# Kernel optimization log

Hardware: AMD Instinct MI355X
Metric: run time of the kernel (lower is better)

## Reference

```python
import jax, jax.numpy as jnp
import numpy as np

B, L, E = 2, 2048, 1024
H = 16
DH = E // H  # head dim for qk and v (dim_qk=dim_v=embed_dim)
HID = 4 * E  # fcn_dim_factor * dim_v
SCALE = DH ** 0.5


def setup_inputs() -> dict:
    key = jax.random.key(0)
    ks = jax.random.split(key, 12)
    s = lambda fan_in: 1.0 / np.sqrt(fan_in)
    return {
        "x": jax.random.uniform(ks[0], (B, L), jnp.float32),
        "z": jax.random.normal(ks[1], (B, L, E), jnp.float32),
        "Wq": jax.random.normal(ks[2], (E, E), jnp.float32) * s(E),
        "bq": jnp.zeros((E,), jnp.float32),
        "Wk": jax.random.normal(ks[3], (E, E), jnp.float32) * s(E),
        "bk": jnp.zeros((E,), jnp.float32),
        "Wv": jax.random.normal(ks[4], (E, E), jnp.float32) * s(E),
        "bv": jnp.zeros((E,), jnp.float32),
        "W1": jax.random.normal(ks[5], (E, HID), jnp.float32) * s(E),
        "b1": jnp.zeros((HID,), jnp.float32),
        "W2": jax.random.normal(ks[6], (HID, 1), jnp.float32) * s(HID),
        "b2": jnp.zeros((1,), jnp.float32),
    }


def reference(x, z, Wq, bq, Wk, bk, Wv, bv, W1, b1, W2, b2):
    # Projections -> (B, H, L, DH)
    def heads(t):
        return t.reshape(B, L, H, DH).transpose(0, 2, 1, 3)

    Q = heads(z @ Wq + bq)
    K = heads(z @ Wk + bk)
    V = heads(z @ Wv + bv)

    # Scores (B, H, L, L)
    S = jnp.einsum("bhid,bhjd->bhij", Q, K) / SCALE

    # Weighted softmax along query axis (dim=-2), weighted by population x
    w = x[:, None, :, None]  # (B, 1, L, 1), broadcasts over queries i
    m = jnp.max(S, axis=-2, keepdims=True)
    e = w * jnp.exp(S - m)
    A = e / jnp.sum(e, axis=-2, keepdims=True)

    # V scaled by population weight, then AV
    V_scaled = w * V
    O = jnp.einsum("bhij,bhjd->bhid", A, V_scaled)  # (B, H, L, DH)
    O = O.transpose(0, 2, 1, 3).reshape(B, L, H * DH)

    # FFN: Linear -> GELU (exact) -> Linear(->1) -> squeeze
    y = jax.nn.gelu(O @ W1 + b1, approximate=False)
    y = (y @ W2 + b2).squeeze(-1)  # (B, L)
    return y
```

## Files before the change

### kernel.cpp

```cpp
#include <hip/hip_runtime.h>
#include <hip/hip_bf16.h>
#include <math.h>

#define B_    2
#define L_    2048
#define E_    1024
#define H_    16
#define DH_   64
#define HID_  4096
#define NROW_ (B_*L_)
#define BH_   (B_*H_)

#define QSCL  0.18033688011112042f

typedef __attribute__((ext_vector_type(8)))  short    short8v;
typedef _Float16 half8v __attribute__((ext_vector_type(8)));
typedef __attribute__((ext_vector_type(16))) float    f32x16;

#define MFMA32(A, Bv, C) __builtin_amdgcn_mfma_f32_32x32x16_bf16((A), (Bv), (C), 0, 0, 0)
#define MFMAH(A, Bv, C)  __builtin_amdgcn_mfma_f32_32x32x16_f16((A), (Bv), (C), 0, 0, 0)

#define WAITV(N) asm volatile("s_waitcnt vmcnt(" #N ")" ::: "memory")
#define SBAR()   __builtin_amdgcn_s_barrier()

__device__ __forceinline__ unsigned short f2bf(float f) {
    union { float f; unsigned u; } v; v.f = f;
    return (unsigned short)((v.u + 0x8000u) >> 16);
}
__device__ __forceinline__ unsigned pack2_bf16(float lo, float hi) {
    union { float f; unsigned u; } a, b; a.f = lo; b.f = hi;
    return __builtin_amdgcn_perm(b.u + 0x8000u, a.u + 0x8000u, 0x07060302u);
}
__device__ __forceinline__ float bf2f(unsigned short u) {
    union { unsigned u; float f; } v; v.u = ((unsigned)u) << 16;
    return v.f;
}

__device__ __forceinline__ void gl_lds16(const void* g, void* l) {
    __builtin_amdgcn_global_load_lds(
        (const __attribute__((address_space(1))) unsigned int*)g,
        (__attribute__((address_space(3))) unsigned int*)l, 16, 0, 0);
}

__device__ __forceinline__ float erf_fast(float v) {
    float a = fabsf(v);
    float t = __builtin_amdgcn_rcpf(1.0f + 0.3275911f * a);
    float p = t * (0.254829592f + t * (-0.284496736f + t * (1.421413741f +
              t * (-1.453152027f + t * 1.061405429f))));
    float r = 1.0f - p * __expf(-a * a);
    return copysignf(r, v);
}

__global__ __launch_bounds__(256) void zh_prep(
    const float* __restrict__ z, _Float16* __restrict__ zh)
{
    const size_t i = ((size_t)blockIdx.x * 256 + threadIdx.x) * 8;
    float4 a = *(const float4*)&z[i];
    float4 b = *(const float4*)&z[i + 4];
    union { _Float16 h[8]; half8v v; } o;
    o.h[0] = (_Float16)a.x; o.h[1] = (_Float16)a.y;
    o.h[2] = (_Float16)a.z; o.h[3] = (_Float16)a.w;
    o.h[4] = (_Float16)b.x; o.h[5] = (_Float16)b.y;
    o.h[6] = (_Float16)b.z; o.h[7] = (_Float16)b.w;
    *(half8v*)&zh[i] = o.v;
}

__global__ __launch_bounds__(256) void wprep3(
    const float* __restrict__ Wq, const float* __restrict__ Wk,
    const float* __restrict__ Wv,
    _Float16* __restrict__ Tq, _Float16* __restrict__ Tk,
    _Float16* __restrict__ Tv)
{
    const float* src = (blockIdx.z == 0) ? Wq : (blockIdx.z == 1) ? Wk : Wv;
    _Float16*    dst = (blockIdx.z == 0) ? Tq : (blockIdx.z == 1) ? Tk : Tv;
    __shared__ float tile[64][65];
    const int t  = threadIdx.x;
    const int r0 = blockIdx.y * 64, c0 = blockIdx.x * 64;
    #pragma unroll
    for (int u = 0; u < 4; ++u) {
        int f = t + 256 * u, row = f >> 4, c4 = (f & 15) << 2;
        *(float4*)&tile[row][c4] = *(const float4*)&src[(size_t)(r0 + row) * E_ + c0 + c4];
    }
    __syncthreads();
    #pragma unroll
    for (int u = 0; u < 4; ++u) {
        int f = t + 256 * u, c = f >> 4, r4 = (f & 15) << 2;
        union { _Float16 h[4]; uint2 u2; } pk;
        pk.h[0] = (_Float16)tile[r4 + 0][c];
        pk.h[1] = (_Float16)tile[r4 + 1][c];
        pk.h[2] = (_Float16)tile[r4 + 2][c];
        pk.h[3] = (_Float16)tile[r4 + 3][c];
        *(uint2*)&dst[(size_t)(c0 + c) * E_ + r0 + r4] = pk.u2;
    }
}

__global__ __launch_bounds__(256) void w1prep(
    const float* __restrict__ W1, _Float16* __restrict__ W1t)
{
    __shared__ float tile[64][65];
    const int t  = threadIdx.x;
    const int r0 = blockIdx.y * 64, c0 = blockIdx.x * 64;
    #pragma unroll
    for (int u = 0; u < 4; ++u) {
        int f = t + 256 * u, row = f >> 4, c4 = (f & 15) << 2;
        *(float4*)&tile[row][c4] = *(const float4*)&W1[(size_t)(r0 + row) * HID_ + c0 + c4];
    }
    __syncthreads();
    #pragma unroll
    for (int u = 0; u < 4; ++u) {
        int f = t + 256 * u, c = f >> 4, r4 = (f & 15) << 2;
        union { _Float16 h[4]; uint2 u2; } pk;
        pk.h[0] = (_Float16)tile[r4 + 0][c];
        pk.h[1] = (_Float16)tile[r4 + 1][c];
        pk.h[2] = (_Float16)tile[r4 + 2][c];
        pk.h[3] = (_Float16)tile[r4 + 3][c];
        *(uint2*)&W1t[(size_t)(c0 + c) * E_ + r0 + r4] = pk.u2;
    }
}

__global__ __launch_bounds__(256) void qkv_mfma(
    const _Float16* __restrict__ zh,
    const _Float16* __restrict__ Tq, const _Float16* __restrict__ Tk,
    const _Float16* __restrict__ Tv,
    const float* __restrict__ bq, const float* __restrict__ bk,
    const float* __restrict__ bv,
    unsigned short* __restrict__ Qo, unsigned short* __restrict__ Ko,
    unsigned short* __restrict__ Vo)
{
    const int which = blockIdx.z;
    const _Float16* Wt = (which == 0) ? Tq : (which == 1) ? Tk : Tv;
    const float*  bias = (which == 0) ? bq : (which == 1) ? bk : bv;
    unsigned short* out = (which == 0) ? Qo : (which == 1) ? Ko : Vo;
    const float   osc  = (which == 0) ? QSCL : 1.0f;

    __shared__ _Float16 Ah[2][128 * 64];
    __shared__ _Float16 Bs[2][128 * 64];

    const int t    = threadIdx.x;
    const int lane = t & 63;
    const int w    = t >> 6;
    const int l31  = lane & 31;
    const int hq   = lane >> 5;
    const int wm   = w >> 1, wn = w & 1;
    const int m0   = blockIdx.x * 128;
    const int n0   = blockIdx.y * 128;

    const int srow0 = (lane >> 3);
    const int ssl   = lane & 7;

    f32x16 acc[2][2] = {};

#define QKV_STAGE(bb, kc)                                                          \
    {                                                                              \
        _Pragma("unroll")                                                          \
        for (int u = 0; u < 4; ++u) {                                              \
            int ch  = w * 4 + u;                                                   \
            int row = ch * 8 + srow0;                                              \
            gl_lds16(&zh[(size_t)(m0 + row) * E_ + (kc) * 64 + ((ssl ^ (row & 7)) << 3)], \
                     &Ah[bb][ch * 512]);                                           \
            gl_lds16(&Wt[(size_t)(n0 + row) * E_ + (kc) * 64 + ((ssl ^ (row & 7)) << 3)], \
                     &Bs[bb][ch * 512]);                                           \
        }                                                                          \
    }

    QKV_STAGE(0, 0);
    QKV_STAGE(1, 1);
    __syncthreads();
    int cur = 0;

    for (int kc = 0; kc < 16; ++kc) {
        if (kc < 15) WAITV(8); else WAITV(0);
        SBAR();
        __builtin_amdgcn_s_setprio(1);
        #pragma unroll
        for (int ks = 0; ks < 4; ++ks) {
            half8v fb[2];
            #pragma unroll
            for (int nb = 0; nb < 2; ++nb) {
                int br = wn * 64 + nb * 32 + l31;
                fb[nb] = *(const half8v*)&Bs[cur][br * 64 + (((ks * 2 + hq) ^ (br & 7)) << 3)];
            }
            #pragma unroll
            for (int mb = 0; mb < 2; ++mb) {
                int ar = wm * 64 + mb * 32 + l31;
                half8v fa = *(const half8v*)&Ah[cur][ar * 64 + (((ks * 2 + hq) ^ (ar & 7)) << 3)];
                acc[mb][0] = MFMAH(fa, fb[0], acc[mb][0]);
                acc[mb][1] = MFMAH(fa, fb[1], acc[mb][1]);
            }
        }
        __builtin_amdgcn_s_setprio(0);
        SBAR();
        if (kc + 2 < 16) QKV_STAGE(cur, kc + 2);
        cur ^= 1;
    }

    #pragma unroll
    for (int nb = 0; nb < 2; ++nb) {
        int n  = n0 + wn * 64 + nb * 32 + l31;
        int h  = n >> 6, dh = n & 63;
        float bb = bias[n];
        #pragma unroll
        for (int mb = 0; mb < 2; ++mb) {
            #pragma unroll
            for (int r = 0; r < 16; ++r) {
                int m  = m0 + wm * 64 + mb * 32 + (r & 3) + 8 * (r >> 2) + 4 * hq;
                int b  = m >> 11, i = m & (L_ - 1);
                out[((size_t)(b * H_ + h) * L_ + i) * DH_ + dh] = f2bf((acc[mb][nb][r] + bb) * osc);
            }
        }
    }
#undef QKV_STAGE
}

__global__ __launch_bounds__(256) void col_stats_mfma(
    const unsigned short* __restrict__ Qb, const unsigned short* __restrict__ Kb,
    const float* __restrict__ x, float* __restrict__ Do)
{
    __shared__ unsigned short Qlds[2][128 * 64];
    __shared__ float xlds[L_];

    const int t    = threadIdx.x;
    const int lane = t & 63;
    const int wv   = t >> 6;
    const int l31  = lane & 31;
    const int hq   = lane >> 5;
    const int bh   = blockIdx.y;
    const int b    = bh >> 4;
    const int j0   = blockIdx.x * 128 + wv * 32;

    const int srow0 = (lane >> 3);
    const int ssl   = lane & 7;

    #pragma unroll
    for (int u = 0; u < 2; ++u) {
        int f = t + 256 * u;
        *(float4*)&xlds[f * 4] = *(const float4*)&x[(size_t)b * L_ + f * 4];
    }

    short8v kf[4];
    {
        const unsigned short* kp = Kb + ((size_t)bh * L_ + j0 + l31) * DH_ + hq * 8;
        #pragma unroll
        for (int c = 0; c < 4; ++c) kf[c] = *(const short8v*)(kp + c * 16);
    }

    float d[16];
    #pragma unroll
    for (int r = 0; r < 16; ++r) d[r] = 0.f;

#define CS_STAGE(bb, ich)                                                           \
    {                                                                               \
        _Pragma("unroll")                                                           \
        for (int u = 0; u < 4; ++u) {                                               \
            int ch  = wv * 4 + u;                                                   \
            int row = ch * 8 + srow0;                                               \
            gl_lds16(&Qb[((size_t)bh * L_ + (ich) * 128 + row) * DH_ + ((ssl ^ (row & 7)) << 3)], \
                     &Qlds[bb][ch * 512]);                                          \
        }                                                                           \
    }

    CS_STAGE(0, 0);
    CS_STAGE(1, 1);
    __syncthreads();
    int cur = 0;

    const int NT = L_ / 128;
    for (int ich = 0; ich < NT; ++ich) {
        if (ich < NT - 1) WAITV(4); else WAITV(0);
        SBAR();
        #pragma unroll
        for (int cc = 0; cc < 4; ++cc) {
            f32x16 acc = {};
            __builtin_amdgcn_s_setprio(1);
            #pragma unroll
            for (int c = 0; c < 4; ++c) {
                int qr = cc * 32 + l31;
                short8v qv = *(const short8v*)&Qlds[cur][qr * 64 + (((c * 2 + hq) ^ (qr & 7)) << 3)];
                acc = MFMA32(kf[c], qv, acc);
            }
            __builtin_amdgcn_s_setprio(0);
            float xi = xlds[ich * 128 + cc * 32 + l31];
            #pragma unroll
            for (int r = 0; r < 16; ++r)
                d[r] += xi * __builtin_amdgcn_exp2f(acc[r]);
        }
        SBAR();
        if (ich + 2 < NT) CS_STAGE(cur, ich + 2);
        cur ^= 1;
    }

    #pragma unroll
    for (int r = 0; r < 16; ++r) {
        #pragma unroll
        for (int off = 16; off > 0; off >>= 1)
            d[r] += __shfl_xor(d[r], off);
    }
    if (l31 == 0) {
        #pragma unroll
        for (int r = 0; r < 16; ++r)
            Do[(size_t)bh * L_ + j0 + 4 * hq + (r & 3) + 8 * (r >> 2)] = d[r];
    }
#undef CS_STAGE
}

__global__ __launch_bounds__(256) void vt_prep(
    const unsigned short* __restrict__ Vb, const float* __restrict__ x,
    const float* __restrict__ Do, unsigned short* __restrict__ Vt)
{
    const int bh = blockIdx.y;
    const int b  = bh >> 4;
    const int j  = blockIdx.x * 256 + threadIdx.x;
    const float s = x[(size_t)b * L_ + j] / Do[(size_t)bh * L_ + j];
    const unsigned short* vp = Vb + ((size_t)bh * L_ + j) * DH_;
    #pragma unroll
    for (int c = 0; c < 16; ++c) {
        ushort4 v = *(const ushort4*)&vp[c * 4];
        Vt[((size_t)bh * DH_ + c * 4 + 0) * L_ + j] = f2bf(bf2f(v.x) * s);
        Vt[((size_t)bh * DH_ + c * 4 + 1) * L_ + j] = f2bf(bf2f(v.y) * s);
        Vt[((size_t)bh * DH_ + c * 4 + 2) * L_ + j] = f2bf(bf2f(v.z) * s);
        Vt[((size_t)bh * DH_ + c * 4 + 3) * L_ + j] = f2bf(bf2f(v.w) * s);
    }
}

__global__ __launch_bounds__(256) void attn_out_mfma(
    const unsigned short* __restrict__ Qb, const unsigned short* __restrict__ Kb,
    const unsigned short* __restrict__ Vt, const float* __restrict__ x,
    _Float16* __restrict__ Of)
{
    __shared__ unsigned short Klds[2][64 * 64];
    __shared__ unsigned short Vlds[2][64 * 64];

    const int t    = threadIdx.x;
    const int lane = t & 63;
    const int wv   = t >> 6;
    const int l31  = lane & 31;
    const int hq   = lane >> 5;
    const int bh   = blockIdx.y;
    const int b    = bh >> 4, hh = bh & 15;
    const int iw   = blockIdx.x * 128 + wv * 32;

    const int srow0 = (lane >> 3);
    const int ssl   = lane & 7;

    short8v qf[4];
    {
        const unsigned short* qp = Qb + ((size_t)bh * L_ + iw + l31) * DH_ + hq * 8;
        #pragma unroll
        for (int c = 0; c < 4; ++c) qf[c] = *(const short8v*)(qp + c * 16);
    }

    f32x16 accO0 = {}, accO1 = {};

#define AO_STAGE(bb, jt)                                                            \
    {                                                                               \
        _Pragma("unroll")                                                           \
        for (int u = 0; u < 2; ++u) {                                               \
            int ch  = wv * 2 + u;                                                   \
            int row = ch * 8 + srow0;                                               \
            gl_lds16(&Kb[((size_t)bh * L_ + (jt) * 64 + row) * DH_ + ((ssl ^ (row & 7)) << 3)], \
                     &Klds[bb][ch * 512]);                                          \
            gl_lds16(&Vt[((size_t)bh * DH_ + row) * L_ + (jt) * 64 + ((ssl ^ (row & 7)) << 3)], \
                     &Vlds[bb][ch * 512]);                                          \
        }                                                                           \
    }

    AO_STAGE(0, 0);
    AO_STAGE(1, 1);
    __syncthreads();
    int cur = 0;

    const int NT = L_ / 64;
    for (int jt = 0; jt < NT; ++jt) {
        if (jt < NT - 1) WAITV(4); else WAITV(0);
        SBAR();

        uint4 pa[4];
        #pragma unroll
        for (int js = 0; js < 2; ++js) {
            f32x16 as = {};
            __builtin_amdgcn_s_setprio(1);
            #pragma unroll
            for (int c = 0; c < 4; ++c) {
                int krow = js * 32 + l31;
                short8v kfr = *(const short8v*)&Klds[cur][krow * 64 + (((c * 2 + hq) ^ (krow & 7)) << 3)];
                as = MFMA32(kfr, qf[c], as);
            }
            __builtin_amdgcn_s_setprio(0);
            float p[16];
            #pragma unroll
            for (int r = 0; r < 16; ++r) p[r] = __builtin_amdgcn_exp2f(as[r]);

            unsigned P0 = pack2_bf16(p[0], p[1]);
            unsigned P1 = pack2_bf16(p[2], p[3]);
            unsigned Q0 = pack2_bf16(p[4], p[5]);
            unsigned Q1 = pack2_bf16(p[6], p[7]);
            asm("v_permlane32_swap_b32 %0, %1" : "+v"(P0), "+v"(Q0));
            asm("v_permlane32_swap_b32 %0, %1" : "+v"(P1), "+v"(Q1));
            pa[js * 2 + 0] = make_uint4(P0, P1, Q0, Q1);

            unsigned R0 = pack2_bf16(p[8],  p[9]);
            unsigned R1 = pack2_bf16(p[10], p[11]);
            unsigned S0 = pack2_bf16(p[12], p[13]);
            unsigned S1 = pack2_bf16(p[14], p[15]);
            asm("v_permlane32_swap_b32 %0, %1" : "+v"(R0), "+v"(S0));
            asm("v_permlane32_swap_b32 %0, %1" : "+v"(R1), "+v"(S1));
            pa[js * 2 + 1] = make_uint4(R0, R1, S0, S1);
        }

        __builtin_amdgcn_s_setprio(1);
        #pragma unroll
        for (int c = 0; c < 4; ++c) {
            union { uint4 u; short8v s; } paf; paf.u = pa[c];
            int r0 = l31, r1 = 32 + l31;
            short8v vf0 = *(const short8v*)&Vlds[cur][r0 * 64 + (((c * 2 + hq) ^ (r0 & 7)) << 3)];
            short8v vf1 = *(const short8v*)&Vlds[cur][r1 * 64 + (((c * 2 + hq) ^ (r1 & 7)) << 3)];
            accO0 = MFMA32(paf.s, vf0, accO0);
            accO1 = MFMA32(paf.s, vf1, accO1);
        }
        __builtin_amdgcn_s_setprio(0);
        SBAR();
        if (jt + 2 < NT) AO_STAGE(cur, jt + 2);
        cur ^= 1;
    }

    #pragma unroll
    for (int q = 0; q < 4; ++q) {
        float4 xq = *(const float4*)&x[(size_t)b * L_ + iw + 4 * hq + 8 * q];
        const float xs[4] = { xq.x, xq.y, xq.z, xq.w };
        #pragma unroll
        for (int k = 0; k < 4; ++k) {
            int r    = q * 4 + k;
            int irow = iw + 4 * hq + 8 * q + k;
            size_t base = ((size_t)b * L_ + irow) * E_ + hh * DH_;
            Of[base + l31]      = (_Float16)(accO0[r] * xs[k]);
            Of[base + 32 + l31] = (_Float16)(accO1[r] * xs[k]);
        }
    }
#undef AO_STAGE
}

__global__ __launch_bounds__(256) void y_init(float* __restrict__ y, const float* __restrict__ b2)
{
    y[blockIdx.x * 256 + threadIdx.x] = b2[0];
}

__global__ __launch_bounds__(256) void mlp_mfma(
    const _Float16* __restrict__ Of, const _Float16* __restrict__ W1t,
    const float* __restrict__ b1, const float* __restrict__ W2,
    float* __restrict__ y)
{
    __shared__ _Float16 Oh[2][128 * 64];
    __shared__ _Float16 Wh[2][128 * 64];

    const int t    = threadIdx.x;
    const int lane = t & 63;
    const int w    = t >> 6;
    const int l31  = lane & 31;
    const int hq   = lane >> 5;
    const int wm   = w >> 1, wn = w & 1;
    const int m0   = blockIdx.x * 128;
    const int n0   = blockIdx.y * 128;

    const int srow0 = (lane >> 3);
    const int ssl   = lane & 7;

    f32x16 acc[2][2] = {};

#define MLP_STAGE(bb, kc)                                                          \
    {                                                                              \
        _Pragma("unroll")                                                          \
        for (int u = 0; u < 4; ++u) {                                              \
            int ch  = w * 4 + u;                                                   \
            int row = ch * 8 + srow0;                                              \
            gl_lds16(&Of[(size_t)(m0 + row) * E_ + (kc) * 64 + ((ssl ^ (row & 7)) << 3)], \
                     &Oh[bb][ch * 512]);                                           \
            gl_lds16(&W1t[(size_t)(n0 + row) * E_ + (kc) * 64 + ((ssl ^ (row & 7)) << 3)], \
                     &Wh[bb][ch * 512]);                                           \
        }                                                                          \
    }

    MLP_STAGE(0, 0);
    MLP_STAGE(1, 1);
    __syncthreads();
    int cur = 0;

    for (int kc = 0; kc < 16; ++kc) {
        if (kc < 15) WAITV(8); else WAITV(0);
        SBAR();
        __builtin_amdgcn_s_setprio(1);
        #pragma unroll
        for (int ks = 0; ks < 4; ++ks) {
            half8v fb[2];
            #pragma unroll
            for (int nb = 0; nb < 2; ++nb) {
                int br = wn * 64 + nb * 32 + l31;
                fb[nb] = *(const half8v*)&Wh[cur][br * 64 + (((ks * 2 + hq) ^ (br & 7)) << 3)];
            }
            #pragma unroll
            for (int mb = 0; mb < 2; ++mb) {
                int ar = wm * 64 + mb * 32 + l31;
                half8v fa = *(const half8v*)&Oh[cur][ar * 64 + (((ks * 2 + hq) ^ (ar & 7)) << 3)];
                acc[mb][0] = MFMAH(fa, fb[0], acc[mb][0]);
                acc[mb][1] = MFMAH(fa, fb[1], acc[mb][1]);
            }
        }
        __builtin_amdgcn_s_setprio(0);
        SBAR();
        if (kc + 2 < 16) MLP_STAGE(cur, kc + 2);
        cur ^= 1;
    }

    const int hid0 = n0 + wn * 64 + l31;
    const float bb0 = b1[hid0],      w20 = W2[hid0];
    const float bb1 = b1[hid0 + 32], w21 = W2[hid0 + 32];
    #pragma unroll
    for (int mb = 0; mb < 2; ++mb) {
        #pragma unroll
        for (int r = 0; r < 16; ++r) {
            float h0 = acc[mb][0][r] + bb0;
            float h1 = acc[mb][1][r] + bb1;
            float s  = 0.5f * h0 * (1.0f + erf_fast(h0 * 0.70710678f)) * w20
                     + 0.5f * h1 * (1.0f + erf_fast(h1 * 0.70710678f)) * w21;
            #pragma unroll
            for (int off = 16; off > 0; off >>= 1) s += __shfl_xor(s, off);
            if (l31 == 0) {
                int m = m0 + wm * 64 + mb * 32 + (r & 3) + 8 * (r >> 2) + 4 * hq;
                atomicAdd(&y[m], s);
            }
        }
    }
#undef MLP_STAGE
}

extern "C" void kernel_launch(void* const* d_in, const int* in_sizes, int n_in,
                              void* d_out, int out_size, void* d_ws, size_t ws_size,
                              hipStream_t stream)
{
    const float* x  = (const float*)d_in[0];
    const float* z  = (const float*)d_in[1];
    const float* Wq = (const float*)d_in[2];
    const float* bq = (const float*)d_in[3];
    const float* Wk = (const float*)d_in[4];
    const float* bk = (const float*)d_in[5];
    const float* Wv = (const float*)d_in[6];
    const float* bv = (const float*)d_in[7];
    const float* W1 = (const float*)d_in[8];
    const float* b1 = (const float*)d_in[9];
    const float* W2 = (const float*)d_in[10];
    const float* b2 = (const float*)d_in[11];
    float* y = (float*)d_out;

    const size_t NQ = (size_t)BH_ * L_ * DH_;
    unsigned short* p = (unsigned short*)d_ws;
    unsigned short* Qb  = p;  p += NQ;
    unsigned short* Kb  = p;  p += NQ;
    unsigned short* Vb  = p;  p += NQ;
    unsigned short* Vt  = p;  p += NQ;
    _Float16* zh  = (_Float16*)p;  p += (size_t)NROW_ * E_;
    _Float16* Tq  = (_Float16*)p;  p += (size_t)E_ * E_;
    _Float16* Tk  = (_Float16*)p;  p += (size_t)E_ * E_;
    _Float16* Tv  = (_Float16*)p;  p += (size_t)E_ * E_;
    _Float16* W1t = (_Float16*)p;  p += (size_t)HID_ * E_;
    _Float16* Ofp = (_Float16*)p;  p += (size_t)NROW_ * E_;
    float* Dw = (float*)p;

    zh_prep<<<dim3((NROW_ * E_) / (256 * 8)), 256, 0, stream>>>(z, zh);
    wprep3 <<<dim3(E_ / 64, E_ / 64, 3), 256, 0, stream>>>(Wq, Wk, Wv, Tq, Tk, Tv);
    w1prep <<<dim3(HID_ / 64, E_ / 64), 256, 0, stream>>>(W1, W1t);

    qkv_mfma<<<dim3(NROW_ / 128, E_ / 128, 3), 256, 0, stream>>>(
        zh, Tq, Tk, Tv, bq, bk, bv, Qb, Kb, Vb);

    col_stats_mfma<<<dim3(L_ / 128, BH_), 256, 0, stream>>>(Qb, Kb, x, Dw);

    vt_prep<<<dim3(L_ / 256, BH_), 256, 0, stream>>>(Vb, x, Dw, Vt);

    attn_out_mfma<<<dim3(L_ / 128, BH_), 256, 0, stream>>>(Qb, Kb, Vt, x, Ofp);

    y_init<<<dim3(NROW_ / 256), 256, 0, stream>>>(y, b2);

    mlp_mfma<<<dim3(NROW_ / 128, HID_ / 128), 256, 0, stream>>>(
        Ofp, W1t, b1, W2, y);
}
```

Baseline: 207.5 us.

## Enlarge MLP and column-stats tiles and flatten QKV weights into one buffer

```diff
diff --git a/kernel.cpp b/kernel.cpp
--- a/kernel.cpp
+++ b/kernel.cpp
@@ -120,18 +120,15 @@
 
 __global__ __launch_bounds__(256) void qkv_mfma(
     const _Float16* __restrict__ zh,
-    const _Float16* __restrict__ Tq, const _Float16* __restrict__ Tk,
-    const _Float16* __restrict__ Tv,
+    const _Float16* __restrict__ Tall,
     const float* __restrict__ bq, const float* __restrict__ bk,
     const float* __restrict__ bv,
-    unsigned short* __restrict__ Qo, unsigned short* __restrict__ Ko,
-    unsigned short* __restrict__ Vo)
-{
-    const int which = blockIdx.z;
-    const _Float16* Wt = (which == 0) ? Tq : (which == 1) ? Tk : Tv;
-    const float*  bias = (which == 0) ? bq : (which == 1) ? bk : bv;
-    unsigned short* out = (which == 0) ? Qo : (which == 1) ? Ko : Vo;
-    const float   osc  = (which == 0) ? QSCL : 1.0f;
+    unsigned short* __restrict__ outQKV)
+{
+    const int which = blockIdx.y >> 3;
+    const float* bias = (which == 0) ? bq : (which == 1) ? bk : bv;
+    const float  osc  = (which == 0) ? QSCL : 1.0f;
+    unsigned short* out = outQKV + (size_t)which * ((size_t)BH_ * L_ * DH_);
 
     __shared__ _Float16 Ah[2][128 * 64];
     __shared__ _Float16 Bs[2][128 * 64];
@@ -158,7 +155,7 @@
             int row = ch * 8 + srow0;                                              \
             gl_lds16(&zh[(size_t)(m0 + row) * E_ + (kc) * 64 + ((ssl ^ (row & 7)) << 3)], \
                      &Ah[bb][ch * 512]);                                           \
-            gl_lds16(&Wt[(size_t)(n0 + row) * E_ + (kc) * 64 + ((ssl ^ (row & 7)) << 3)], \
+            gl_lds16(&Tall[(size_t)(n0 + row) * E_ + (kc) * 64 + ((ssl ^ (row & 7)) << 3)], \
                      &Bs[bb][ch * 512]);                                           \
         }                                                                          \
     }
@@ -197,8 +194,9 @@
     #pragma unroll
     for (int nb = 0; nb < 2; ++nb) {
         int n  = n0 + wn * 64 + nb * 32 + l31;
-        int h  = n >> 6, dh = n & 63;
-        float bb = bias[n];
+        int nn = n & 1023;
+        int h  = nn >> 6, dh = nn & 63;
+        float bb = bias[nn];
         #pragma unroll
         for (int mb = 0; mb < 2; ++mb) {
             #pragma unroll
@@ -226,7 +224,7 @@
     const int hq   = lane >> 5;
     const int bh   = blockIdx.y;
     const int b    = bh >> 4;
-    const int j0   = blockIdx.x * 128 + wv * 32;
+    const int j0   = blockIdx.x * 256 + wv * 64;
 
     const int srow0 = (lane >> 3);
     const int ssl   = lane & 7;
@@ -237,16 +235,17 @@
         *(float4*)&xlds[f * 4] = *(const float4*)&x[(size_t)b * L_ + f * 4];
     }
 
-    short8v kf[4];
-    {
-        const unsigned short* kp = Kb + ((size_t)bh * L_ + j0 + l31) * DH_ + hq * 8;
-        #pragma unroll
-        for (int c = 0; c < 4; ++c) kf[c] = *(const short8v*)(kp + c * 16);
-    }
-
-    float d[16];
-    #pragma unroll
-    for (int r = 0; r < 16; ++r) d[r] = 0.f;
+    short8v kf[2][4];
+    #pragma unroll
+    for (int s = 0; s < 2; ++s) {
+        const unsigned short* kp = Kb + ((size_t)bh * L_ + j0 + s * 32 + l31) * DH_ + hq * 8;
+        #pragma unroll
+        for (int c = 0; c < 4; ++c) kf[s][c] = *(const short8v*)(kp + c * 16);
+    }
+
+    float d0[16], d1[16];
+    #pragma unroll
+    for (int r = 0; r < 16; ++r) { d0[r] = 0.f; d1[r] = 0.f; }
 
 #define CS_STAGE(bb, ich)                                                           \
     {                                                                               \
@@ -270,19 +269,22 @@
         SBAR();
         #pragma unroll
         for (int cc = 0; cc < 4; ++cc) {
-            f32x16 acc = {};
+            f32x16 a0 = {}, a1 = {};
             __builtin_amdgcn_s_setprio(1);
             #pragma unroll
             for (int c = 0; c < 4; ++c) {
                 int qr = cc * 32 + l31;
                 short8v qv = *(const short8v*)&Qlds[cur][qr * 64 + (((c * 2 + hq) ^ (qr & 7)) << 3)];
-                acc = MFMA32(kf[c], qv, acc);
+                a0 = MFMA32(kf[0][c], qv, a0);
+                a1 = MFMA32(kf[1][c], qv, a1);
             }
             __builtin_amdgcn_s_setprio(0);
             float xi = xlds[ich * 128 + cc * 32 + l31];
             #pragma unroll
-            for (int r = 0; r < 16; ++r)
-                d[r] += xi * __builtin_amdgcn_exp2f(acc[r]);
+            for (int r = 0; r < 16; ++r) {
+                d0[r] += xi * __builtin_amdgcn_exp2f(a0[r]);
+                d1[r] += xi * __builtin_amdgcn_exp2f(a1[r]);
+            }
         }
         SBAR();
         if (ich + 2 < NT) CS_STAGE(cur, ich + 2);
@@ -292,13 +294,18 @@
     #pragma unroll
     for (int r = 0; r < 16; ++r) {
         #pragma unroll
-        for (int off = 16; off > 0; off >>= 1)
-            d[r] += __shfl_xor(d[r], off);
+        for (int off = 16; off > 0; off >>= 1) {
+            d0[r] += __shfl_xor(d0[r], off);
+            d1[r] += __shfl_xor(d1[r], off);
+        }
     }
     if (l31 == 0) {
         #pragma unroll
-        for (int r = 0; r < 16; ++r)
-            Do[(size_t)bh * L_ + j0 + 4 * hq + (r & 3) + 8 * (r >> 2)] = d[r];
+        for (int r = 0; r < 16; ++r) {
+            int jr = 4 * hq + (r & 3) + 8 * (r >> 2);
+            Do[(size_t)bh * L_ + j0 + jr]      = d0[r];
+            Do[(size_t)bh * L_ + j0 + 32 + jr] = d1[r];
+        }
     }
 #undef CS_STAGE
 }
@@ -444,27 +451,27 @@
     y[blockIdx.x * 256 + threadIdx.x] = b2[0];
 }
 
-__global__ __launch_bounds__(256) void mlp_mfma(
+__global__ __launch_bounds__(512) void mlp_mfma(
     const _Float16* __restrict__ Of, const _Float16* __restrict__ W1t,
     const float* __restrict__ b1, const float* __restrict__ W2,
     float* __restrict__ y)
 {
-    __shared__ _Float16 Oh[2][128 * 64];
-    __shared__ _Float16 Wh[2][128 * 64];
+    __shared__ _Float16 Oh[2][256 * 64];
+    __shared__ _Float16 Wh[2][256 * 64];
 
     const int t    = threadIdx.x;
     const int lane = t & 63;
     const int w    = t >> 6;
     const int l31  = lane & 31;
     const int hq   = lane >> 5;
-    const int wm   = w >> 1, wn = w & 1;
-    const int m0   = blockIdx.x * 128;
-    const int n0   = blockIdx.y * 128;
+    const int wm   = w >> 2, wn = w & 3;
+    const int m0   = blockIdx.x * 256;
+    const int n0   = blockIdx.y * 256;
 
     const int srow0 = (lane >> 3);
     const int ssl   = lane & 7;
 
-    f32x16 acc[2][2] = {};
+    f32x16 acc[4][2] = {};
 
 #define MLP_STAGE(bb, kc)                                                          \
     {                                                                              \
@@ -497,8 +504,8 @@
                 fb[nb] = *(const half8v*)&Wh[cur][br * 64 + (((ks * 2 + hq) ^ (br & 7)) << 3)];
             }
             #pragma unroll
-            for (int mb = 0; mb < 2; ++mb) {
-                int ar = wm * 64 + mb * 32 + l31;
+            for (int mb = 0; mb < 4; ++mb) {
+                int ar = wm * 128 + mb * 32 + l31;
                 half8v fa = *(const half8v*)&Oh[cur][ar * 64 + (((ks * 2 + hq) ^ (ar & 7)) << 3)];
                 acc[mb][0] = MFMAH(fa, fb[0], acc[mb][0]);
                 acc[mb][1] = MFMAH(fa, fb[1], acc[mb][1]);
@@ -514,7 +521,7 @@
     const float bb0 = b1[hid0],      w20 = W2[hid0];
     const float bb1 = b1[hid0 + 32], w21 = W2[hid0 + 32];
     #pragma unroll
-    for (int mb = 0; mb < 2; ++mb) {
+    for (int mb = 0; mb < 4; ++mb) {
         #pragma unroll
         for (int r = 0; r < 16; ++r) {
             float h0 = acc[mb][0][r] + bb0;
@@ -524,7 +531,7 @@
             #pragma unroll
             for (int off = 16; off > 0; off >>= 1) s += __shfl_xor(s, off);
             if (l31 == 0) {
-                int m = m0 + wm * 64 + mb * 32 + (r & 3) + 8 * (r >> 2) + 4 * hq;
+                int m = m0 + wm * 128 + mb * 32 + (r & 3) + 8 * (r >> 2) + 4 * hq;
                 atomicAdd(&y[m], s);
             }
         }
@@ -568,10 +575,10 @@
     wprep3 <<<dim3(E_ / 64, E_ / 64, 3), 256, 0, stream>>>(Wq, Wk, Wv, Tq, Tk, Tv);
     w1prep <<<dim3(HID_ / 64, E_ / 64), 256, 0, stream>>>(W1, W1t);
 
-    qkv_mfma<<<dim3(NROW_ / 128, E_ / 128, 3), 256, 0, stream>>>(
-        zh, Tq, Tk, Tv, bq, bk, bv, Qb, Kb, Vb);
-
-    col_stats_mfma<<<dim3(L_ / 128, BH_), 256, 0, stream>>>(Qb, Kb, x, Dw);
+    qkv_mfma<<<dim3(NROW_ / 128, 3 * E_ / 128), 256, 0, stream>>>(
+        zh, Tq, bq, bk, bv, Qb);
+
+    col_stats_mfma<<<dim3(L_ / 256, BH_), 256, 0, stream>>>(Qb, Kb, x, Dw);
 
     vt_prep<<<dim3(L_ / 256, BH_), 256, 0, stream>>>(Vb, x, Dw, Vt);
 
@@ -579,6 +586,6 @@
 
     y_init<<<dim3(NROW_ / 256), 256, 0, stream>>>(y, b2);
 
-    mlp_mfma<<<dim3(NROW_ / 128, HID_ / 128), 256, 0, stream>>>(
+    mlp_mfma<<<dim3(NROW_ / 256, HID_ / 256), 512, 0, stream>>>(
         Ofp, W1t, b1, W2, y);
 }
```

New measurement: 221.8 us. 1.07x slower.
